# Optimization experiments

Measured on AMD Instinct MI355X. Metric: run time of the kernel, lower is better.

## Reference

```python
import jax, jax.numpy as jnp
import numpy as np

N, A, D, E = 524288, 8, 64, 32
LOG2PI = float(np.log(2.0 * np.pi))


def setup_inputs() -> dict:
    key = jax.random.key(0)
    ks = jax.random.split(key, 6)
    return {
        "state": jax.random.normal(ks[0], (N, D), jnp.float32),
        "W": jax.random.normal(ks[1], (A, D, E), jnp.float32) * 0.05,
        "b": jax.random.normal(ks[2], (A, E), jnp.float32) * 0.05,
        "log_std": jax.random.normal(ks[3], (A, E), jnp.float32) * 0.1,
        "eps": jax.random.normal(ks[4], (N, E), jnp.float32),
        "actor_indices": jax.random.randint(ks[5], (N,), 0, A, dtype=jnp.int32),
    }


def reference(state, W, b, log_std, eps, actor_indices):
    # Dispatch: stable sort samples by routed actor (mirrors the per-actor
    # boolean-mask gather + concat, which produces group-major, stable order).
    p = jnp.argsort(actor_indices)            # [N] original index of k-th sorted sample
    s_state = state[p]                        # [N, D] states in actor-grouped order
    s_idx = actor_indices[p]                  # [N] sorted actor ids

    # Per-actor linear-Gaussian policy, selected per sample.
    mean_all = jnp.einsum('nd,ade->nae', s_state, W) + b          # [N, A, E]
    mean = jnp.take_along_axis(mean_all, s_idx[:, None, None], axis=1)[:, 0, :]  # [N, E]
    ls = log_std[s_idx]                                           # [N, E]
    std = jnp.exp(ls)

    # rsample + log_prob (summed over action dim), eps consumed in group order
    action = mean + std * eps                                     # [N, E]
    lp = jnp.sum(-0.5 * ((action - mean) / std) ** 2 - ls - 0.5 * LOG2PI, axis=-1)  # [N]

    # Combine exactly as the source: combined[argsort(actor_indices)]
    # (indexes the group-ordered concat by the forward permutation).
    return action[p], lp[p]
```

## Files before the change

### kernel.cpp

```cpp
#include <hip/hip_runtime.h>
#include <math.h>

#define N_SAMPLES 524288
#define A_ACT 8
#define D_DIM 64
#define E_DIM 32
#define LOG2PI_F 1.8378770664093453f

#define SORT_THREADS 256
#define CHUNK 1024
#define NBLK (N_SAMPLES / CHUNK)
#define HIST_SIZE (A_ACT * NBLK)
#define SCAN_PER (HIST_SIZE / 256)

typedef __attribute__((ext_vector_type(8))) short bf16x8;
typedef __attribute__((ext_vector_type(4))) float f32x4;

__device__ __forceinline__ short f2bf(float f) {
  unsigned u = __float_as_uint(f);
  unsigned r = (u + 0x7FFFu + ((u >> 16) & 1u)) >> 16;
  return (short)r;
}

__global__ __launch_bounds__(SORT_THREADS) void hist_kernel(
    const int* __restrict__ idx, int* __restrict__ hist) {
  __shared__ int cnt[A_ACT];
  int t = threadIdx.x;
  if (t < A_ACT) cnt[t] = 0;
  __syncthreads();
  int base = blockIdx.x * CHUNK;
#pragma unroll
  for (int j = 0; j < CHUNK / SORT_THREADS; ++j) {
    atomicAdd(&cnt[idx[base + j * SORT_THREADS + t]], 1);
  }
  __syncthreads();
  if (t < A_ACT) hist[t * NBLK + blockIdx.x] = cnt[t];
}

__global__ __launch_bounds__(256) void scan_kernel(int* __restrict__ hist) {
  __shared__ int sums[256];
  int t = threadIdx.x;
  int vals[SCAN_PER];
  int s = 0;
#pragma unroll
  for (int k = 0; k < SCAN_PER; ++k) {
    vals[k] = hist[t * SCAN_PER + k];
    s += vals[k];
  }
  sums[t] = s;
  __syncthreads();
  for (int off = 1; off < 256; off <<= 1) {
    int v = (t >= off) ? sums[t - off] : 0;
    __syncthreads();
    sums[t] += v;
    __syncthreads();
  }
  int prefix = (t == 0) ? 0 : sums[t - 1];
#pragma unroll
  for (int k = 0; k < SCAN_PER; ++k) {
    int v = vals[k];
    hist[t * SCAN_PER + k] = prefix;
    prefix += v;
  }
}

__global__ __launch_bounds__(SORT_THREADS) void scatter_kernel(
    const int* __restrict__ idx, const int* __restrict__ offs,
    int* __restrict__ p, int* __restrict__ inv) {
  __shared__ int base[A_ACT];
  __shared__ int wcnt[4][A_ACT];
  int t = threadIdx.x;
  int wave = t >> 6;
  int lane = t & 63;
  if (t < A_ACT) base[t] = offs[t * NBLK + blockIdx.x];
  __syncthreads();
  int cstart = blockIdx.x * CHUNK;
#pragma unroll
  for (int pass = 0; pass < CHUNK / SORT_THREADS; ++pass) {
    int i = cstart + pass * SORT_THREADS + t;
    int a = idx[i];
    unsigned long long mymask = 0ULL;
#pragma unroll
    for (int aa = 0; aa < A_ACT; ++aa) {
      unsigned long long m = __ballot(a == aa);
      if (aa == a) mymask = m;
      if (lane == 0) wcnt[wave][aa] = __popcll(m);
    }
    unsigned long long below = (1ULL << lane) - 1ULL;
    int inwave = __popcll(mymask & below);
    __syncthreads();
    int wprefix = 0;
#pragma unroll
    for (int w = 0; w < 4; ++w)
      if (w < wave) wprefix += wcnt[w][a];
    int r = base[a] + wprefix + inwave;
    p[r] = i;
    inv[i] = r;
    __syncthreads();
    if (t < A_ACT) {
      int tot = 0;
#pragma unroll
      for (int w = 0; w < 4; ++w) tot += wcnt[w][t];
      base[t] += tot;
    }
    __syncthreads();
  }
}

#define TILE_ROWS 128
#define MAIN_THREADS 256
#define MAIN_BLOCKS (N_SAMPLES / TILE_ROWS + A_ACT)

__global__ __launch_bounds__(MAIN_THREADS, 6) void main_kernel(
    const float* __restrict__ state, const float* __restrict__ W,
    const float* __restrict__ bias, const float* __restrict__ lstd,
    const float* __restrict__ eps, const int* __restrict__ p,
    const int* __restrict__ inv, const int* __restrict__ offs,
    float* __restrict__ out_action, float* __restrict__ out_lp) {
  __shared__ short sA[TILE_ROWS * D_DIM];
  __shared__ short sB[E_DIM * D_DIM];
  __shared__ int s_d[TILE_ROWS];

  int t = threadIdx.x;
  int bid = blockIdx.x;

  int a = -1, kbase = 0, kend = 0;
  int acc_b = 0;
#pragma unroll
  for (int aa = 0; aa < A_ACT; ++aa) {
    int start = offs[aa * NBLK];
    int end = (aa == A_ACT - 1) ? N_SAMPLES : offs[(aa + 1) * NBLK];
    int cnt = end - start;
    int nc = (cnt + TILE_ROWS - 1) / TILE_ROWS;
    if (a < 0 && bid < acc_b + nc) {
      a = aa;
      int chunk = bid - acc_b;
      kbase = start + chunk * TILE_ROWS;
      kend = min(end, kbase + TILE_ROWS);
    }
    acc_b += nc;
  }
  if (a < 0) return;
  int nrows = kend - kbase;

  if (t < TILE_ROWS) s_d[t] = inv[kbase + min(t, nrows - 1)];

  {
    int col = t >> 3;
    int kc = t & 7;
    const float* wp = W + (size_t)a * (D_DIM * E_DIM) + (kc * 8) * E_DIM + col;
    bf16x8 v;
#pragma unroll
    for (int j = 0; j < 8; ++j) v[j] = f2bf(wp[j * E_DIM]);
    *(bf16x8*)(&sB[col * D_DIM + ((kc ^ (col & 7)) << 3)]) = v;
  }

  {
    int u = t >> 4;
    int x = t & 15;
    int pm[TILE_ROWS / 16];
#pragma unroll
    for (int it = 0; it < TILE_ROWS / 16; ++it) {
      int row = it * 16 + u;
      pm[it] = p[kbase + min(row, nrows - 1)];
    }
#pragma unroll
    for (int it = 0; it < TILE_ROWS / 16; ++it) {
      int row = it * 16 + u;
      float4 v = *(const float4*)(state + (size_t)pm[it] * D_DIM + x * 4);
      unsigned lo = ((unsigned)(unsigned short)f2bf(v.y) << 16) |
                    (unsigned)(unsigned short)f2bf(v.x);
      unsigned hi = ((unsigned)(unsigned short)f2bf(v.w) << 16) |
                    (unsigned)(unsigned short)f2bf(v.z);
      int soff = row * D_DIM + (((x >> 1) ^ (row & 7)) << 3) + ((x & 1) << 2);
      *(uint2*)(&sA[soff]) = make_uint2(lo, hi);
    }
  }
  __syncthreads();

  int w = t >> 6;
  int l = t & 63;
  int lrow = l & 15;
  int lk = l >> 4;

  f32x4 acc[2][2];
#pragma unroll
  for (int rt = 0; rt < 2; ++rt)
#pragma unroll
    for (int ct = 0; ct < 2; ++ct) acc[rt][ct] = (f32x4){0.f, 0.f, 0.f, 0.f};

#pragma unroll
  for (int ks = 0; ks < 2; ++ks) {
    int kc = ks * 4 + lk;
    bf16x8 aF[2], bF[2];
#pragma unroll
    for (int rt = 0; rt < 2; ++rt) {
      int row = w * 32 + rt * 16 + lrow;
      aF[rt] = *(const bf16x8*)(&sA[row * D_DIM + ((kc ^ (row & 7)) << 3)]);
    }
#pragma unroll
    for (int ct = 0; ct < 2; ++ct) {
      int col = ct * 16 + lrow;
      bF[ct] = *(const bf16x8*)(&sB[col * D_DIM + ((kc ^ (col & 7)) << 3)]);
    }
#pragma unroll
    for (int rt = 0; rt < 2; ++rt)
#pragma unroll
      for (int ct = 0; ct < 2; ++ct)
        acc[rt][ct] = __builtin_amdgcn_mfma_f32_16x16x32_bf16(
            aF[rt], bF[ct], acc[rt][ct], 0, 0, 0);
  }

  __syncthreads();

  float* sC = (float*)sA;
#pragma unroll
  for (int rt = 0; rt < 2; ++rt) {
#pragma unroll
    for (int ct = 0; ct < 2; ++ct) {
      int col = ct * 16 + lrow;
#pragma unroll
      for (int r = 0; r < 4; ++r) {
        int row = w * 32 + rt * 16 + lk * 4 + r;
        sC[row * E_DIM + (((col >> 2) ^ (row & 7)) << 2) + (col & 3)] =
            acc[rt][ct][r];
      }
    }
  }
  __syncthreads();

  int c = t & 7;
  float4 bv = *(const float4*)(bias + a * E_DIM + c * 4);
  float4 lv = *(const float4*)(lstd + a * E_DIM + c * 4);
  const float bva[4] = {bv.x, bv.y, bv.z, bv.w};
  const float lsa[4] = {lv.x, lv.y, lv.z, lv.w};
  float sda[4];
#pragma unroll
  for (int j = 0; j < 4; ++j) sda[j] = expf(lsa[j]);
  float lsum = lsa[0] + lsa[1] + lsa[2] + lsa[3];

#pragma unroll
  for (int pass = 0; pass < TILE_ROWS / 32; ++pass) {
    int row = pass * 32 + (t >> 3);
    bool valid = (row < nrows);
    int rc = valid ? row : (nrows - 1);
    int krc = kbase + rc;
    int dest = s_d[rc];
    float4 ev = *(const float4*)(eps + (size_t)krc * E_DIM + c * 4);
    float4 av = *(const float4*)(&sC[row * E_DIM + ((c ^ (row & 7)) << 2)]);
    const float ep[4] = {ev.x, ev.y, ev.z, ev.w};
    const float ac[4] = {av.x, av.y, av.z, av.w};
    float o[4];
    float part = -lsum;
#pragma unroll
    for (int j = 0; j < 4; ++j) {
      o[j] = fmaf(sda[j], ep[j], ac[j] + bva[j]);
      part = fmaf(-0.5f * ep[j], ep[j], part);
    }
    part += __shfl_xor(part, 1, 64);
    part += __shfl_xor(part, 2, 64);
    part += __shfl_xor(part, 4, 64);
    if (valid) {
      *(float4*)(&out_action[(size_t)dest * E_DIM + c * 4]) =
          make_float4(o[0], o[1], o[2], o[3]);
      if (c == 0) out_lp[dest] = part - 16.0f * LOG2PI_F;
    }
  }
}

extern "C" void kernel_launch(void* const* d_in, const int* in_sizes, int n_in,
                              void* d_out, int out_size, void* d_ws, size_t ws_size,
                              hipStream_t stream) {
  const float* state = (const float*)d_in[0];
  const float* W     = (const float*)d_in[1];
  const float* b     = (const float*)d_in[2];
  const float* ls    = (const float*)d_in[3];
  const float* eps   = (const float*)d_in[4];
  const int*   idx   = (const int*)d_in[5];

  float* out_action = (float*)d_out;
  float* out_lp     = (float*)d_out + (size_t)N_SAMPLES * E_DIM;

  int* p    = (int*)d_ws;
  int* inv  = p + N_SAMPLES;
  int* hist = inv + N_SAMPLES;

  hipLaunchKernelGGL(hist_kernel, dim3(NBLK), dim3(SORT_THREADS), 0, stream,
                     idx, hist);
  hipLaunchKernelGGL(scan_kernel, dim3(1), dim3(256), 0, stream, hist);
  hipLaunchKernelGGL(scatter_kernel, dim3(NBLK), dim3(SORT_THREADS), 0, stream,
                     idx, hist, p, inv);
  hipLaunchKernelGGL(main_kernel, dim3(MAIN_BLOCKS), dim3(MAIN_THREADS),
                     0, stream, state, W, b, ls, eps, p, inv, hist,
                     out_action, out_lp);
}
```

Before: 63.38 us.

## Load gathered state rows directly into MFMA A-fragments and prefetch eps early

The main kernel no longer stages the gathered state tile through shared memory. Each lane loads the fp32 state values it needs for its MFMA A operand straight into registers and packs them to bf16 there. Eps values, inverse-permutation destinations, bias and log_std are all issued before the barrier so their global loads overlap. One barrier goes away, LDS use shrinks, and the launch-bounds occupancy hint drops from 6 to 4. The sort chunk size is also halved, which doubles the histogram and scan size. The extra registers held live may lower occupancy.

```diff
diff --git a/kernel.cpp b/kernel.cpp
--- a/kernel.cpp
+++ b/kernel.cpp
@@ -8,7 +8,7 @@
 #define LOG2PI_F 1.8378770664093453f
 
 #define SORT_THREADS 256
-#define CHUNK 1024
+#define CHUNK 512
 #define NBLK (N_SAMPLES / CHUNK)
 #define HIST_SIZE (A_ACT * NBLK)
 #define SCAN_PER (HIST_SIZE / 256)
@@ -20,6 +20,13 @@
   unsigned u = __float_as_uint(f);
   unsigned r = (u + 0x7FFFu + ((u >> 16) & 1u)) >> 16;
   return (short)r;
+}
+
+__device__ __forceinline__ bf16x8 pack8(float4 a, float4 b) {
+  bf16x8 r;
+  r[0] = f2bf(a.x); r[1] = f2bf(a.y); r[2] = f2bf(a.z); r[3] = f2bf(a.w);
+  r[4] = f2bf(b.x); r[5] = f2bf(b.y); r[6] = f2bf(b.z); r[7] = f2bf(b.w);
+  return r;
 }
 
 __global__ __launch_bounds__(SORT_THREADS) void hist_kernel(
@@ -111,15 +118,14 @@
 #define MAIN_THREADS 256
 #define MAIN_BLOCKS (N_SAMPLES / TILE_ROWS + A_ACT)
 
-__global__ __launch_bounds__(MAIN_THREADS, 6) void main_kernel(
+__global__ __launch_bounds__(MAIN_THREADS, 4) void main_kernel(
     const float* __restrict__ state, const float* __restrict__ W,
     const float* __restrict__ bias, const float* __restrict__ lstd,
     const float* __restrict__ eps, const int* __restrict__ p,
     const int* __restrict__ inv, const int* __restrict__ offs,
     float* __restrict__ out_action, float* __restrict__ out_lp) {
-  __shared__ short sA[TILE_ROWS * D_DIM];
   __shared__ short sB[E_DIM * D_DIM];
-  __shared__ int s_d[TILE_ROWS];
+  __shared__ float sC[TILE_ROWS * E_DIM];
 
   int t = threadIdx.x;
   int bid = blockIdx.x;
@@ -143,8 +149,6 @@
   if (a < 0) return;
   int nrows = kend - kbase;
 
-  if (t < TILE_ROWS) s_d[t] = inv[kbase + min(t, nrows - 1)];
-
   {
     int col = t >> 3;
     int kc = t & 7;
@@ -155,33 +159,42 @@
     *(bf16x8*)(&sB[col * D_DIM + ((kc ^ (col & 7)) << 3)]) = v;
   }
 
-  {
-    int u = t >> 4;
-    int x = t & 15;
-    int pm[TILE_ROWS / 16];
-#pragma unroll
-    for (int it = 0; it < TILE_ROWS / 16; ++it) {
-      int row = it * 16 + u;
-      pm[it] = p[kbase + min(row, nrows - 1)];
-    }
-#pragma unroll
-    for (int it = 0; it < TILE_ROWS / 16; ++it) {
-      int row = it * 16 + u;
-      float4 v = *(const float4*)(state + (size_t)pm[it] * D_DIM + x * 4);
-      unsigned lo = ((unsigned)(unsigned short)f2bf(v.y) << 16) |
-                    (unsigned)(unsigned short)f2bf(v.x);
-      unsigned hi = ((unsigned)(unsigned short)f2bf(v.w) << 16) |
-                    (unsigned)(unsigned short)f2bf(v.z);
-      int soff = row * D_DIM + (((x >> 1) ^ (row & 7)) << 3) + ((x & 1) << 2);
-      *(uint2*)(&sA[soff]) = make_uint2(lo, hi);
-    }
-  }
-  __syncthreads();
-
   int w = t >> 6;
   int l = t & 63;
   int lrow = l & 15;
   int lk = l >> 4;
+  int r0 = w * 32;
+
+  int mrow[2];
+#pragma unroll
+  for (int rt = 0; rt < 2; ++rt)
+    mrow[rt] = p[kbase + min(r0 + rt * 16 + lrow, nrows - 1)];
+
+  float4 av[2][2][2];
+#pragma unroll
+  for (int rt = 0; rt < 2; ++rt) {
+#pragma unroll
+    for (int ks = 0; ks < 2; ++ks) {
+      const float* sp = state + (size_t)mrow[rt] * D_DIM + ks * 32 + lk * 8;
+      av[rt][ks][0] = *(const float4*)sp;
+      av[rt][ks][1] = *(const float4*)(sp + 4);
+    }
+  }
+
+  int c = t & 7;
+  float4 epv[4];
+  int dst[4];
+#pragma unroll
+  for (int pass = 0; pass < 4; ++pass) {
+    int row = pass * 32 + (t >> 3);
+    int rc = min(row, nrows - 1);
+    epv[pass] = *(const float4*)(eps + (size_t)(kbase + rc) * E_DIM + c * 4);
+    dst[pass] = inv[kbase + rc];
+  }
+  float4 bv = *(const float4*)(bias + a * E_DIM + c * 4);
+  float4 lv = *(const float4*)(lstd + a * E_DIM + c * 4);
+
+  __syncthreads();
 
   f32x4 acc[2][2];
 #pragma unroll
@@ -194,10 +207,8 @@
     int kc = ks * 4 + lk;
     bf16x8 aF[2], bF[2];
 #pragma unroll
-    for (int rt = 0; rt < 2; ++rt) {
-      int row = w * 32 + rt * 16 + lrow;
-      aF[rt] = *(const bf16x8*)(&sA[row * D_DIM + ((kc ^ (row & 7)) << 3)]);
-    }
+    for (int rt = 0; rt < 2; ++rt)
+      aF[rt] = pack8(av[rt][ks][0], av[rt][ks][1]);
 #pragma unroll
     for (int ct = 0; ct < 2; ++ct) {
       int col = ct * 16 + lrow;
@@ -211,9 +222,6 @@
             aF[rt], bF[ct], acc[rt][ct], 0, 0, 0);
   }
 
-  __syncthreads();
-
-  float* sC = (float*)sA;
 #pragma unroll
   for (int rt = 0; rt < 2; ++rt) {
 #pragma unroll
@@ -221,7 +229,7 @@
       int col = ct * 16 + lrow;
 #pragma unroll
       for (int r = 0; r < 4; ++r) {
-        int row = w * 32 + rt * 16 + lk * 4 + r;
+        int row = r0 + rt * 16 + lk * 4 + r;
         sC[row * E_DIM + (((col >> 2) ^ (row & 7)) << 2) + (col & 3)] =
             acc[rt][ct][r];
       }
@@ -229,9 +237,6 @@
   }
   __syncthreads();
 
-  int c = t & 7;
-  float4 bv = *(const float4*)(bias + a * E_DIM + c * 4);
-  float4 lv = *(const float4*)(lstd + a * E_DIM + c * 4);
   const float bva[4] = {bv.x, bv.y, bv.z, bv.w};
   const float lsa[4] = {lv.x, lv.y, lv.z, lv.w};
   float sda[4];
@@ -240,16 +245,13 @@
   float lsum = lsa[0] + lsa[1] + lsa[2] + lsa[3];
 
 #pragma unroll
-  for (int pass = 0; pass < TILE_ROWS / 32; ++pass) {
+  for (int pass = 0; pass < 4; ++pass) {
     int row = pass * 32 + (t >> 3);
     bool valid = (row < nrows);
-    int rc = valid ? row : (nrows - 1);
-    int krc = kbase + rc;
-    int dest = s_d[rc];
-    float4 ev = *(const float4*)(eps + (size_t)krc * E_DIM + c * 4);
-    float4 av = *(const float4*)(&sC[row * E_DIM + ((c ^ (row & 7)) << 2)]);
-    const float ep[4] = {ev.x, ev.y, ev.z, ev.w};
-    const float ac[4] = {av.x, av.y, av.z, av.w};
+    int rcrow = valid ? row : (nrows - 1);
+    float4 av2 = *(const float4*)(&sC[rcrow * E_DIM + ((c ^ (rcrow & 7)) << 2)]);
+    const float ep[4] = {epv[pass].x, epv[pass].y, epv[pass].z, epv[pass].w};
+    const float ac[4] = {av2.x, av2.y, av2.z, av2.w};
     float o[4];
     float part = -lsum;
 #pragma unroll
@@ -261,9 +263,9 @@
     part += __shfl_xor(part, 2, 64);
     part += __shfl_xor(part, 4, 64);
     if (valid) {
-      *(float4*)(&out_action[(size_t)dest * E_DIM + c * 4]) =
+      *(float4*)(&out_action[(size_t)dst[pass] * E_DIM + c * 4]) =
           make_float4(o[0], o[1], o[2], o[3]);
-      if (c == 0) out_lp[dest] = part - 16.0f * LOG2PI_F;
+      if (c == 0) out_lp[dst[pass]] = part - 16.0f * LOG2PI_F;
     }
   }
 }
```

After: 65.08 us. 2.7% more time.
